# Kernel tuning notes

Hardware: AMD Instinct MI355X
Metric: run time of the kernel (lower is better)

Reference implementation:

```python
import jax, jax.numpy as jnp
import numpy as np

N = 8192      # nodes
R = 3         # relations
D_IN = 64
D_HID = 64
D_OUT = 64


def setup_inputs() -> dict:
    key = jax.random.key(0)
    ks = jax.random.split(key, 6)
    x = jax.random.normal(ks[0], (N, D_IN), dtype=jnp.float32)
    # dense normalized adjacency-hat per relation; 1/N scale keeps tanh unsaturated
    adj = jax.random.uniform(ks[1], (R, N, N), dtype=jnp.float32) * (1.0 / N)
    s1 = 1.0 / np.sqrt(D_IN)
    s2 = 1.0 / np.sqrt(D_HID)
    W1 = jax.random.uniform(ks[2], (R, D_IN, D_HID), dtype=jnp.float32, minval=-s1, maxval=s1)
    b1 = jax.random.uniform(ks[3], (R, D_HID), dtype=jnp.float32, minval=-s1, maxval=s1)
    W2 = jax.random.uniform(ks[4], (R, D_HID, D_OUT), dtype=jnp.float32, minval=-s2, maxval=s2)
    b2 = jax.random.uniform(ks[5], (R, D_OUT), dtype=jnp.float32, minval=-s2, maxval=s2)
    return {"x": x, "adj": adj, "W1": W1, "b1": b1, "W2": W2, "b2": b2}


def _relgcn_conv(x, adj, W, b):
    # per-relation linear: [R, N, d_out]
    h = jnp.einsum('nf,rfh->rnh', x, W) + b[:, None, :]
    # adjacency matmul per relation, summed over relations: [N, d_out]
    m = jnp.einsum('rnm,rmh->nh', adj, h)
    return jnp.tanh(m)


def reference(x, adj, W1, b1, W2, b2):
    h = _relgcn_conv(x, adj, W1, b1)   # layer 0: in -> hidden
    y = _relgcn_conv(h, adj, W2, b2)   # layer 1: hidden -> out
    return y
```

## Files before the change

### kernel.cpp

```cpp
#include <hip/hip_runtime.h>


#define NN 8192
#define TS 516

typedef __attribute__((ext_vector_type(4))) float float4v;
typedef __attribute__((ext_vector_type(8))) short short8v;
typedef __attribute__((ext_vector_type(4))) int int4v;

__device__ inline unsigned short f2bf(float f) {
  unsigned int u = __builtin_bit_cast(unsigned int, f);
  return (unsigned short)((u + 0x7FFFu + ((u >> 16) & 1u)) >> 16);
}

__device__ inline float tri_dither(unsigned int e) {
  unsigned int s = e * 2654435761u;
  s ^= s >> 16;
  s *= 2246822519u;
  s ^= s >> 13;
  return ((float)((s & 0xffffu) + (s >> 16)) * (1.f / 65536.f)) - 1.f;
}

__global__ __launch_bounds__(256) void prep(
    const float* __restrict__ in, const float* __restrict__ W,
    const float* __restrict__ b, unsigned short* __restrict__ hbf) {
  __shared__ float Ws[64 * 64];
  const int tid = threadIdx.x;
  const int r = blockIdx.x >> 8;
  const int g = blockIdx.x & 255;
  const int ml = tid >> 3;
  const int j0 = (tid & 7) * 8;
  const int m = g * 32 + ml;
#pragma unroll
  for (int i = 0; i < 16; ++i) Ws[tid + i * 256] = W[r * 4096 + tid + i * 256];
  float4v xr[16];
#pragma unroll
  for (int i = 0; i < 16; ++i) xr[i] = *(const float4v*)&in[(size_t)m * 64 + i * 4];
  float acc[8];
  {
    const float4v b0 = *(const float4v*)&b[r * 64 + j0];
    const float4v b1 = *(const float4v*)&b[r * 64 + j0 + 4];
#pragma unroll
    for (int jj = 0; jj < 4; ++jj) { acc[jj] = b0[jj]; acc[jj + 4] = b1[jj]; }
  }
  __syncthreads();
#pragma unroll
  for (int fi = 0; fi < 16; ++fi) {
    const float4v xv = xr[fi];
#pragma unroll
    for (int df = 0; df < 4; ++df) {
      const int f = fi * 4 + df;
      const float a = xv[df];
      const float4v w0 = *(const float4v*)&Ws[f * 64 + j0];
      const float4v w1 = *(const float4v*)&Ws[f * 64 + j0 + 4];
#pragma unroll
      for (int jj = 0; jj < 4; ++jj) {
        acc[jj] += a * w0[jj];
        acc[jj + 4] += a * w1[jj];
      }
    }
  }
  const size_t base = ((size_t)(r * 1024 + (m >> 3)) * 64) * 8 + (m & 7);
#pragma unroll
  for (int jj = 0; jj < 8; ++jj)
    hbf[base + (size_t)(j0 + jj) * 8] = f2bf(acc[jj]);
}

__global__ __launch_bounds__(256) void prep_q(
    const float* __restrict__ in, const float* __restrict__ W,
    const float* __restrict__ b, unsigned char* __restrict__ hq, float S) {
  __shared__ float Ws[64 * 64];
  const int tid = threadIdx.x;
  const int r = blockIdx.x >> 8;
  const int g = blockIdx.x & 255;
  const int ml = tid >> 3;
  const int j0 = (tid & 7) * 8;
  const int m = g * 32 + ml;
#pragma unroll
  for (int i = 0; i < 16; ++i) Ws[tid + i * 256] = W[r * 4096 + tid + i * 256];
  float4v xr[16];
#pragma unroll
  for (int i = 0; i < 16; ++i) xr[i] = *(const float4v*)&in[(size_t)m * 64 + i * 4];
  float acc[8];
  {
    const float4v b0 = *(const float4v*)&b[r * 64 + j0];
    const float4v b1 = *(const float4v*)&b[r * 64 + j0 + 4];
#pragma unroll
    for (int jj = 0; jj < 4; ++jj) { acc[jj] = b0[jj]; acc[jj + 4] = b1[jj]; }
  }
  __syncthreads();
#pragma unroll
  for (int fi = 0; fi < 16; ++fi) {
    const float4v xv = xr[fi];
#pragma unroll
    for (int df = 0; df < 4; ++df) {
      const int f = fi * 4 + df;
      const float a = xv[df];
      const float4v w0 = *(const float4v*)&Ws[f * 64 + j0];
      const float4v w1 = *(const float4v*)&Ws[f * 64 + j0 + 4];
#pragma unroll
      for (int jj = 0; jj < 4; ++jj) {
        acc[jj] += a * w0[jj];
        acc[jj + 4] += a * w1[jj];
      }
    }
  }
  const size_t base = ((size_t)(r * 1024 + (m >> 3)) * 64) * 8 + (m & 7);
#pragma unroll
  for (int jj = 0; jj < 8; ++jj) {
    float v = acc[jj] * S + tri_dither((unsigned)((r * NN + m) * 64 + j0 + jj));
    int q = (int)rintf(v);
    q = q > 127 ? 127 : (q < -127 ? -127 : q);
    hq[base + (size_t)(j0 + jj) * 8] = (unsigned char)(q & 0xff);
  }
}

__global__ __launch_bounds__(256) void gemm1_emit(
    const float* __restrict__ adj, const unsigned short* __restrict__ hbf,
    float* __restrict__ out, unsigned char* __restrict__ adjq) {
  __shared__ float lds[2 * 16 * TS];
  float* buf0 = lds;
  float* buf1 = lds + 16 * TS;
  const int tid = threadIdx.x;
  const int w = tid >> 6;
  const int l = tid & 63;
  const int lrow = l & 15;
  const int lk = l >> 4;
  const int mb = blockIdx.x;
  const int phase = (mb * 29) % 48;
  const int srow = tid >> 4;
  const int sseg = tid & 15;
  const float* arow = adj + (size_t)(mb * 16 + srow) * NN + sseg * 4;
  unsigned char* a8row = adjq + (size_t)(mb * 16 + srow) * NN + sseg * 4;

  float4v acc0 = {0.f, 0.f, 0.f, 0.f}, acc1 = acc0, acc2 = acc0, acc3 = acc0;
  float4v P0, P1, P2, P3, P4, P5, P6, P7, Q0, Q1, Q2, Q3, Q4, Q5, Q6, Q7;

#define TW(TQ) ((TQ) + phase >= 48 ? (TQ) + phase - 48 : (TQ) + phase)
#define TOFF(T) (((size_t)((T) >> 4) << 26) + ((size_t)((T) & 15) << 9))

#define GLOAD(T, S)                                                            \
  do {                                                                         \
    const float* pa_ = arow + TOFF(T);                                         \
    S##0 = __builtin_nontemporal_load((const float4v*)(pa_));                  \
    S##1 = __builtin_nontemporal_load((const float4v*)(pa_ + 64));             \
    S##2 = __builtin_nontemporal_load((const float4v*)(pa_ + 128));            \
    S##3 = __builtin_nontemporal_load((const float4v*)(pa_ + 192));            \
    S##4 = __builtin_nontemporal_load((const float4v*)(pa_ + 256));            \
    S##5 = __builtin_nontemporal_load((const float4v*)(pa_ + 320));            \
    S##6 = __builtin_nontemporal_load((const float4v*)(pa_ + 384));            \
    S##7 = __builtin_nontemporal_load((const float4v*)(pa_ + 448));            \
  } while (0)

#define Q8ST(S, K)                                                             \
  *(unsigned int*)(q8_ + (K) * 64) =                                           \
      (unsigned)(S[0] * 1040384.f + 0.5f) |                                    \
      ((unsigned)(S[1] * 1040384.f + 0.5f) << 8) |                             \
      ((unsigned)(S[2] * 1040384.f + 0.5f) << 16) |                            \
      ((unsigned)(S[3] * 1040384.f + 0.5f) << 24)

#define DSWRITE(BUF, S, T8)                                                    \
  do {                                                                         \
    float* p_ = (BUF) + srow * TS + sseg * 4;                                  \
    *(float4v*)(p_) = S##0;                                                    \
    *(float4v*)(p_ + 64) = S##1;                                               \
    *(float4v*)(p_ + 128) = S##2;                                              \
    *(float4v*)(p_ + 192) = S##3;                                              \
    *(float4v*)(p_ + 256) = S##4;                                              \
    *(float4v*)(p_ + 320) = S##5;                                              \
    *(float4v*)(p_ + 384) = S##6;                                              \
    *(float4v*)(p_ + 448) = S##7;                                              \
    unsigned char* q8_ = a8row + (T8);                                         \
    Q8ST(S##0, 0); Q8ST(S##1, 1); Q8ST(S##2, 2); Q8ST(S##3, 3);                \
    Q8ST(S##4, 4); Q8ST(S##5, 5); Q8ST(S##6, 6); Q8ST(S##7, 7);                \
  } while (0)

#define DO_CHUNK(CUR, CC, B0, B1, B2, B3)                                      \
  do {                                                                         \
    const float* ap_ = (CUR) + lrow * TS + (w * 4 + (CC)) * 32 + lk * 8;       \
    const float4v a0_ = *(const float4v*)ap_;                                  \
    const float4v a1_ = *(const float4v*)(ap_ + 4);                            \
    short8v av_;                                                               \
    av_[0] = (short)f2bf(a0_[0]); av_[1] = (short)f2bf(a0_[1]);                \
    av_[2] = (short)f2bf(a0_[2]); av_[3] = (short)f2bf(a0_[3]);                \
    av_[4] = (short)f2bf(a1_[0]); av_[5] = (short)f2bf(a1_[1]);                \
    av_[6] = (short)f2bf(a1_[2]); av_[7] = (short)f2bf(a1_[3]);                \
    acc0 = __builtin_amdgcn_mfma_f32_16x16x32_bf16(av_, B0, acc0, 0, 0, 0);    \
    acc1 = __builtin_amdgcn_mfma_f32_16x16x32_bf16(av_, B1, acc1, 0, 0, 0);    \
    acc2 = __builtin_amdgcn_mfma_f32_16x16x32_bf16(av_, B2, acc2, 0, 0, 0);    \
    acc3 = __builtin_amdgcn_mfma_f32_16x16x32_bf16(av_, B3, acc3, 0, 0, 0);    \
  } while (0)

#define TILE(TQ, CBUF, WBUF, WS, LS)                                           \
  do {                                                                         \
    const int T_ = TW(TQ);                                                     \
    const unsigned short* pbb_ =                                               \
        hbf +                                                                  \
        ((size_t)((T_ >> 4) * 1024 + (T_ & 15) * 64 + w * 16 + lk) * 512) +    \
        lrow * 8;                                                              \
    const short8v B00 = *(const short8v*)(pbb_);                               \
    const short8v B01 = *(const short8v*)(pbb_ + 128);                         \
    const short8v B02 = *(const short8v*)(pbb_ + 256);                         \
    const short8v B03 = *(const short8v*)(pbb_ + 384);                         \
    const short8v B10 = *(const short8v*)(pbb_ + 2048);                        \
    const short8v B11 = *(const short8v*)(pbb_ + 2176);                        \
    const short8v B12 = *(const short8v*)(pbb_ + 2304);                        \
    const short8v B13 = *(const short8v*)(pbb_ + 2432);                        \
    const short8v B20 = *(const short8v*)(pbb_ + 4096);                        \
    const short8v B21 = *(const short8v*)(pbb_ + 4224);                        \
    const short8v B22 = *(const short8v*)(pbb_ + 4352);                        \
    const short8v B23 = *(const short8v*)(pbb_ + 4480);                        \
    const short8v B30 = *(const short8v*)(pbb_ + 6144);                        \
    const short8v B31 = *(const short8v*)(pbb_ + 6272);                        \
    const short8v B32 = *(const short8v*)(pbb_ + 6400);                        \
    const short8v B33 = *(const short8v*)(pbb_ + 6528);                        \
    if ((TQ) + 1 < 48) DSWRITE(WBUF, WS, TOFF(TW((TQ) + 1)));                  \
    if ((TQ) + 2 < 48) GLOAD(TW((TQ) + 2), LS);                                \
    DO_CHUNK(CBUF, 0, B00, B01, B02, B03);                                     \
    DO_CHUNK(CBUF, 1, B10, B11, B12, B13);                                     \
    DO_CHUNK(CBUF, 2, B20, B21, B22, B23);                                     \
    DO_CHUNK(CBUF, 3, B30, B31, B32, B33);                                     \
    __syncthreads();                                                           \
  } while (0)

  GLOAD(TW(0), P);
  DSWRITE(buf0, P, TOFF(TW(0)));
  GLOAD(TW(1), Q);
  __syncthreads();

#pragma unroll 1
  for (int tq = 0; tq < 48; tq += 2) {
    TILE(tq, buf0, buf1, Q, P);
    TILE(tq + 1, buf1, buf0, P, Q);
  }
#undef TILE
#undef DO_CHUNK
#undef DSWRITE
#undef Q8ST
#undef GLOAD
#undef TW

  float* red = lds;
#pragma unroll
  for (int q = 0; q < 4; ++q) {
    red[w * 1024 + (lk * 4 + q) * 64 + 0 + lrow] = acc0[q];
    red[w * 1024 + (lk * 4 + q) * 64 + 16 + lrow] = acc1[q];
    red[w * 1024 + (lk * 4 + q) * 64 + 32 + lrow] = acc2[q];
    red[w * 1024 + (lk * 4 + q) * 64 + 48 + lrow] = acc3[q];
  }
  __syncthreads();
#pragma unroll
  for (int idx = tid; idx < 1024; idx += 256) {
    const float s = red[idx] + red[1024 + idx] + red[2048 + idx] + red[3072 + idx];
    out[(size_t)mb * 1024 + idx] = tanhf(s);
  }
}

__global__ __launch_bounds__(512) void gemm2_i8(
    const unsigned char* __restrict__ adjq, const unsigned char* __restrict__ hq,
    float* __restrict__ out, float inv) {
  __shared__ int red[8 * 1024];
  const int tid = threadIdx.x;
  const int w = tid >> 6;
  const int l = tid & 63;
  const int lrow = l & 15;
  const int lk = l >> 4;
  const int mb = blockIdx.x;
  const int poff = (mb * 29) % 96;
  const unsigned char* parow = adjq + (size_t)(mb * 16 + lrow) * NN + lk * 8;

  int4v acc0 = {0, 0, 0, 0}, acc1 = acc0, acc2 = acc0, acc3 = acc0;
  long pA, qA, sA;
  long pB0, pB1, pB2, pB3, qB0, qB1, qB2, qB3, sB0, sB1, sB2, sB3;

#define TW96(IT) ((IT) + poff >= 96 ? (IT) + poff - 96 : (IT) + poff)

#define ISSUE(IT, A, B0, B1, B2, B3)                                           \
  do {                                                                         \
    const int c_ = TW96(IT) * 8 + w;                                           \
    const int r_ = c_ >> 8;                                                    \
    const int mm_ = (c_ & 255) << 5;                                           \
    A = *(const long*)(parow + ((size_t)r_ << 26) + mm_);                      \
    const unsigned char* pb_ =                                                 \
        hq + (size_t)(r_ * 1024 + (mm_ >> 3) + lk) * 512 + lrow * 8;           \
    B0 = *(const long*)(pb_);                                                  \
    B1 = *(const long*)(pb_ + 128);                                            \
    B2 = *(const long*)(pb_ + 256);                                            \
    B3 = *(const long*)(pb_ + 384);                                            \
  } while (0)

#define COMPUTE(A, B0, B1, B2, B3)                                             \
  do {                                                                         \
    acc0 = __builtin_amdgcn_mfma_i32_16x16x32_i8(A, B0, acc0, 0, 0, 0);        \
    acc1 = __builtin_amdgcn_mfma_i32_16x16x32_i8(A, B1, acc1, 0, 0, 0);        \
    acc2 = __builtin_amdgcn_mfma_i32_16x16x32_i8(A, B2, acc2, 0, 0, 0);        \
    acc3 = __builtin_amdgcn_mfma_i32_16x16x32_i8(A, B3, acc3, 0, 0, 0);        \
  } while (0)

  ISSUE(0, pA, pB0, pB1, pB2, pB3);
  ISSUE(1, qA, qB0, qB1, qB2, qB3);
#pragma unroll 1
  for (int it = 0; it < 96; it += 3) {
    ISSUE(it + 2, sA, sB0, sB1, sB2, sB3);
    COMPUTE(pA, pB0, pB1, pB2, pB3);
    if (it + 3 < 96) ISSUE(it + 3, pA, pB0, pB1, pB2, pB3);
    COMPUTE(qA, qB0, qB1, qB2, qB3);
    if (it + 4 < 96) ISSUE(it + 4, qA, qB0, qB1, qB2, qB3);
    COMPUTE(sA, sB0, sB1, sB2, sB3);
  }
#undef ISSUE
#undef COMPUTE
#undef TW96

#pragma unroll
  for (int q = 0; q < 4; ++q) {
    red[w * 1024 + (lk * 4 + q) * 64 + 0 + lrow] = acc0[q];
    red[w * 1024 + (lk * 4 + q) * 64 + 16 + lrow] = acc1[q];
    red[w * 1024 + (lk * 4 + q) * 64 + 32 + lrow] = acc2[q];
    red[w * 1024 + (lk * 4 + q) * 64 + 48 + lrow] = acc3[q];
  }
  __syncthreads();
#pragma unroll
  for (int idx = tid; idx < 1024; idx += 512) {
    int s = 0;
#pragma unroll
    for (int wb = 0; wb < 8; ++wb) s += red[wb * 1024 + idx];
    out[(size_t)mb * 1024 + idx] = tanhf((float)s * inv);
  }
}

__global__ __launch_bounds__(256) void fill_sentinel(float* __restrict__ dst) {
  dst[blockIdx.x * 256 + threadIdx.x] = 7.0f;
}

extern "C" void kernel_launch(void* const* d_in, const int* in_sizes, int n_in,
                              void* d_out, int out_size, void* d_ws, size_t ws_size,
                              hipStream_t stream) {
  const float* x   = (const float*)d_in[0];
  const float* adj = (const float*)d_in[1];
  const float* W1  = (const float*)d_in[2];
  const float* b1  = (const float*)d_in[3];
  const float* W2  = (const float*)d_in[4];
  const float* b2  = (const float*)d_in[5];
  float* out = (float*)d_out;

  const size_t A8_B  = (size_t)3 * 8192 * 8192;
  const size_t HBF_B = (size_t)3 * 8192 * 64 * 2;
  const size_t T_B   = (size_t)8192 * 64 * 4;
  const size_t HQ_B  = (size_t)3 * 8192 * 64;
  if (ws_size < A8_B + HBF_B + T_B + HQ_B) {
    fill_sentinel<<<2048, 256, 0, stream>>>(out);
    return;
  }
  unsigned char* adjq = (unsigned char*)d_ws;
  unsigned short* hbf = (unsigned short*)((char*)d_ws + A8_B);
  float* t            = (float*)((char*)d_ws + A8_B + HBF_B);
  unsigned char* hq   = (unsigned char*)((char*)d_ws + A8_B + HBF_B + T_B);

  prep<<<3 * 256, 256, 0, stream>>>(x, W1, b1, hbf);
  gemm1_emit<<<512, 256, 0, stream>>>(adj, hbf, t, adjq);
  prep_q<<<3 * 256, 256, 0, stream>>>(t, W2, b2, hq, 64.f);
  gemm2_i8<<<512, 512, 0, stream>>>(adjq, hq, out, 1.f / (1040384.f * 64.f));
}
```

Measured before the change: 317.3 us.

## Switch layer-2 int8 GEMM to 16x16x64 MFMA with a fragment-tiled layout

Rewrites the quantized adjacency and hidden-feature layouts into 16-byte MFMA fragment tiles, so gemm2 can issue 128-bit loads and use the 16x16x64 i8 MFMA, halving its loop trip count. The gemm1 emit step now writes adjq in this tiled order. It also adds a single-block probe kernel that checks the new MFMA operand layout against a scalar reference and deliberately stalls if they disagree, which adds an extra launch and a serial dependency.

```diff
diff --git a/kernel.cpp b/kernel.cpp
--- a/kernel.cpp
+++ b/kernel.cpp
@@ -105,13 +105,13 @@
       }
     }
   }
-  const size_t base = ((size_t)(r * 1024 + (m >> 3)) * 64) * 8 + (m & 7);
+  const size_t base = ((size_t)(r * 512 + (m >> 4)) * 64) * 16 + (m & 15);
 #pragma unroll
   for (int jj = 0; jj < 8; ++jj) {
     float v = acc[jj] * S + tri_dither((unsigned)((r * NN + m) * 64 + j0 + jj));
     int q = (int)rintf(v);
     q = q > 127 ? 127 : (q < -127 ? -127 : q);
-    hq[base + (size_t)(j0 + jj) * 8] = (unsigned char)(q & 0xff);
+    hq[base + (size_t)(j0 + jj) * 16] = (unsigned char)(q & 0xff);
   }
 }
 
@@ -131,7 +131,8 @@
   const int srow = tid >> 4;
   const int sseg = tid & 15;
   const float* arow = adj + (size_t)(mb * 16 + srow) * NN + sseg * 4;
-  unsigned char* a8row = adjq + (size_t)(mb * 16 + srow) * NN + sseg * 4;
+  unsigned char* a8base = adjq + (size_t)mb * 384 * 1024 +
+                          (size_t)(srow + 16 * (sseg >> 2)) * 16 + (sseg & 3) * 4;
 
   float4v acc0 = {0.f, 0.f, 0.f, 0.f}, acc1 = acc0, acc2 = acc0, acc3 = acc0;
   float4v P0, P1, P2, P3, P4, P5, P6, P7, Q0, Q1, Q2, Q3, Q4, Q5, Q6, Q7;
@@ -152,14 +153,13 @@
     S##7 = __builtin_nontemporal_load((const float4v*)(pa_ + 448));            \
   } while (0)
 
-#define Q8ST(S, K)                                                             \
-  *(unsigned int*)(q8_ + (K) * 64) =                                           \
-      (unsigned)(S[0] * 1040384.f + 0.5f) |                                    \
-      ((unsigned)(S[1] * 1040384.f + 0.5f) << 8) |                             \
-      ((unsigned)(S[2] * 1040384.f + 0.5f) << 16) |                            \
-      ((unsigned)(S[3] * 1040384.f + 0.5f) << 24)
-
-#define DSWRITE(BUF, S, T8)                                                    \
+#define QPK(S)                                                                 \
+  ((unsigned)(S[0] * 1040384.f + 0.5f) |                                       \
+   ((unsigned)(S[1] * 1040384.f + 0.5f) << 8) |                                \
+   ((unsigned)(S[2] * 1040384.f + 0.5f) << 16) |                               \
+   ((unsigned)(S[3] * 1040384.f + 0.5f) << 24))
+
+#define DSWRITE(BUF, S, T_)                                                    \
   do {                                                                         \
     float* p_ = (BUF) + srow * TS + sseg * 4;                                  \
     *(float4v*)(p_) = S##0;                                                    \
@@ -170,9 +170,16 @@
     *(float4v*)(p_ + 320) = S##5;                                              \
     *(float4v*)(p_ + 384) = S##6;                                              \
     *(float4v*)(p_ + 448) = S##7;                                              \
-    unsigned char* q8_ = a8row + (T8);                                         \
-    Q8ST(S##0, 0); Q8ST(S##1, 1); Q8ST(S##2, 2); Q8ST(S##3, 3);                \
-    Q8ST(S##4, 4); Q8ST(S##5, 5); Q8ST(S##6, 6); Q8ST(S##7, 7);                \
+    unsigned char* q8_ =                                                       \
+        a8base + ((size_t)((T_ >> 4) * 128 + (T_ & 15) * 8)) * 1024;           \
+    *(unsigned*)(q8_) = QPK(S##0);                                             \
+    *(unsigned*)(q8_ + 1024) = QPK(S##1);                                      \
+    *(unsigned*)(q8_ + 2048) = QPK(S##2);                                      \
+    *(unsigned*)(q8_ + 3072) = QPK(S##3);                                      \
+    *(unsigned*)(q8_ + 4096) = QPK(S##4);                                      \
+    *(unsigned*)(q8_ + 5120) = QPK(S##5);                                      \
+    *(unsigned*)(q8_ + 6144) = QPK(S##6);                                      \
+    *(unsigned*)(q8_ + 7168) = QPK(S##7);                                      \
   } while (0)
 
 #define DO_CHUNK(CUR, CC, B0, B1, B2, B3)                                      \
@@ -214,7 +221,7 @@
     const short8v B31 = *(const short8v*)(pbb_ + 6272);                        \
     const short8v B32 = *(const short8v*)(pbb_ + 6400);                        \
     const short8v B33 = *(const short8v*)(pbb_ + 6528);                        \
-    if ((TQ) + 1 < 48) DSWRITE(WBUF, WS, TOFF(TW((TQ) + 1)));                  \
+    if ((TQ) + 1 < 48) DSWRITE(WBUF, WS, TW((TQ) + 1));                        \
     if ((TQ) + 2 < 48) GLOAD(TW((TQ) + 2), LS);                                \
     DO_CHUNK(CBUF, 0, B00, B01, B02, B03);                                     \
     DO_CHUNK(CBUF, 1, B10, B11, B12, B13);                                     \
@@ -224,7 +231,7 @@
   } while (0)
 
   GLOAD(TW(0), P);
-  DSWRITE(buf0, P, TOFF(TW(0)));
+  DSWRITE(buf0, P, TW(0));
   GLOAD(TW(1), Q);
   __syncthreads();
 
@@ -236,7 +243,7 @@
 #undef TILE
 #undef DO_CHUNK
 #undef DSWRITE
-#undef Q8ST
+#undef QPK
 #undef GLOAD
 #undef TW
 
@@ -266,51 +273,50 @@
   const int lrow = l & 15;
   const int lk = l >> 4;
   const int mb = blockIdx.x;
-  const int poff = (mb * 29) % 96;
-  const unsigned char* parow = adjq + (size_t)(mb * 16 + lrow) * NN + lk * 8;
+  const int poff = (mb * 29) % 48;
+  const unsigned char* pabase = adjq + (size_t)mb * 384 * 1024 + l * 16;
 
   int4v acc0 = {0, 0, 0, 0}, acc1 = acc0, acc2 = acc0, acc3 = acc0;
-  long pA, qA, sA;
-  long pB0, pB1, pB2, pB3, qB0, qB1, qB2, qB3, sB0, sB1, sB2, sB3;
-
-#define TW96(IT) ((IT) + poff >= 96 ? (IT) + poff - 96 : (IT) + poff)
+  int4v pA, pB0, pB1, pB2, pB3, qA, qB0, qB1, qB2, qB3, sA, sB0, sB1, sB2, sB3;
+
+#define TW48(IT) ((IT) + poff >= 48 ? (IT) + poff - 48 : (IT) + poff)
 
 #define ISSUE(IT, A, B0, B1, B2, B3)                                           \
   do {                                                                         \
-    const int c_ = TW96(IT) * 8 + w;                                           \
-    const int r_ = c_ >> 8;                                                    \
-    const int mm_ = (c_ & 255) << 5;                                           \
-    A = *(const long*)(parow + ((size_t)r_ << 26) + mm_);                      \
+    const int c_ = TW48(IT) * 8 + w;                  \
+    A = *(const int4v*)(pabase + (size_t)c_ * 1024);                           \
+    const int r_ = c_ >> 7;                                                    \
+    const int mm_ = (c_ & 127) << 6;                                           \
     const unsigned char* pb_ =                                                 \
-        hq + (size_t)(r_ * 1024 + (mm_ >> 3) + lk) * 512 + lrow * 8;           \
-    B0 = *(const long*)(pb_);                                                  \
-    B1 = *(const long*)(pb_ + 128);                                            \
-    B2 = *(const long*)(pb_ + 256);                                            \
-    B3 = *(const long*)(pb_ + 384);                                            \
+        hq + ((size_t)(r_ * 512 + (mm_ >> 4) + lk) * 64 + lrow) * 16;          \
+    B0 = *(const int4v*)(pb_);                                                 \
+    B1 = *(const int4v*)(pb_ + 256);                                           \
+    B2 = *(const int4v*)(pb_ + 512);                                           \
+    B3 = *(const int4v*)(pb_ + 768);                                           \
   } while (0)
 
 #define COMPUTE(A, B0, B1, B2, B3)                                             \
   do {                                                                         \
-    acc0 = __builtin_amdgcn_mfma_i32_16x16x32_i8(A, B0, acc0, 0, 0, 0);        \
-    acc1 = __builtin_amdgcn_mfma_i32_16x16x32_i8(A, B1, acc1, 0, 0, 0);        \
-    acc2 = __builtin_amdgcn_mfma_i32_16x16x32_i8(A, B2, acc2, 0, 0, 0);        \
-    acc3 = __builtin_amdgcn_mfma_i32_16x16x32_i8(A, B3, acc3, 0, 0, 0);        \
+    acc0 = __builtin_amdgcn_mfma_i32_16x16x64_i8(A, B0, acc0, 0, 0, 0);        \
+    acc1 = __builtin_amdgcn_mfma_i32_16x16x64_i8(A, B1, acc1, 0, 0, 0);        \
+    acc2 = __builtin_amdgcn_mfma_i32_16x16x64_i8(A, B2, acc2, 0, 0, 0);        \
+    acc3 = __builtin_amdgcn_mfma_i32_16x16x64_i8(A, B3, acc3, 0, 0, 0);        \
   } while (0)
 
   ISSUE(0, pA, pB0, pB1, pB2, pB3);
   ISSUE(1, qA, qB0, qB1, qB2, qB3);
 #pragma unroll 1
-  for (int it = 0; it < 96; it += 3) {
+  for (int it = 0; it < 48; it += 3) {
     ISSUE(it + 2, sA, sB0, sB1, sB2, sB3);
     COMPUTE(pA, pB0, pB1, pB2, pB3);
-    if (it + 3 < 96) ISSUE(it + 3, pA, pB0, pB1, pB2, pB3);
+    if (it + 3 < 48) ISSUE(it + 3, pA, pB0, pB1, pB2, pB3);
     COMPUTE(qA, qB0, qB1, qB2, qB3);
-    if (it + 4 < 96) ISSUE(it + 4, qA, qB0, qB1, qB2, qB3);
+    if (it + 4 < 48) ISSUE(it + 4, qA, qB0, qB1, qB2, qB3);
     COMPUTE(sA, sB0, sB1, sB2, sB3);
   }
 #undef ISSUE
 #undef COMPUTE
-#undef TW96
+#undef TW48
 
 #pragma unroll
   for (int q = 0; q < 4; ++q) {
@@ -326,6 +332,54 @@
 #pragma unroll
     for (int wb = 0; wb < 8; ++wb) s += red[wb * 1024 + idx];
     out[(size_t)mb * 1024 + idx] = tanhf((float)s * inv);
+  }
+}
+
+__global__ __launch_bounds__(64) void i8_probe(
+    const unsigned char* __restrict__ adjq, const unsigned char* __restrict__ hq) {
+  __shared__ int cm[16 * 64];
+  __shared__ int flag;
+  const int l = threadIdx.x;
+  if (l == 0) flag = 0;
+  const int lrow = l & 15, lk = l >> 4;
+  int4v acc[4];
+#pragma unroll
+  for (int g = 0; g < 4; ++g) acc[g] = (int4v){0, 0, 0, 0};
+#pragma unroll
+  for (int c = 0; c < 2; ++c) {
+    const int4v av = *(const int4v*)&adjq[((size_t)c * 64 + l) * 16];
+#pragma unroll
+    for (int g = 0; g < 4; ++g) {
+      const int4v bv =
+          *(const int4v*)&hq[((size_t)(c * 4 + lk) * 64 + g * 16 + lrow) * 16];
+      acc[g] = __builtin_amdgcn_mfma_i32_16x16x64_i8(av, bv, acc[g], 0, 0, 0);
+    }
+  }
+#pragma unroll
+  for (int g = 0; g < 4; ++g)
+#pragma unroll
+    for (int q = 0; q < 4; ++q)
+      cm[(lk * 4 + q) * 64 + g * 16 + lrow] = acc[g][q];
+  __syncthreads();
+  const int row = l & 15, c0 = (l >> 4) * 16;
+  int bad = 0;
+  for (int cc = 0; cc < 16; ++cc) {
+    const int col = c0 + cc;
+    int ref = 0;
+    for (int k = 0; k < 128; ++k) {
+      const unsigned char a8 =
+          adjq[((size_t)(k >> 6) * 64 + (row & 15) + 16 * ((k >> 4) & 3)) * 16 +
+               (k & 15)];
+      const unsigned char h8 =
+          hq[((size_t)(k >> 4) * 64 + col) * 16 + (k & 15)];
+      ref += (int)a8 * (int)(signed char)h8;
+    }
+    if (cm[row * 64 + col] != ref) bad = 1;
+  }
+  if (bad) atomicOr(&flag, 1);
+  __syncthreads();
+  if (flag) {
+    for (int i = 0; i < 150; ++i) __builtin_amdgcn_s_sleep(127);
   }
 }
 
@@ -360,5 +414,6 @@
   prep<<<3 * 256, 256, 0, stream>>>(x, W1, b1, hbf);
   gemm1_emit<<<512, 256, 0, stream>>>(adj, hbf, t, adjq);
   prep_q<<<3 * 256, 256, 0, stream>>>(t, W2, b2, hq, 64.f);
+  i8_probe<<<1, 64, 0, stream>>>(adjq, hq);
   gemm2_i8<<<512, 512, 0, stream>>>(adjq, hq, out, 1.f / (1040384.f * 64.f));
 }
```

New measurement: 373.2 us. +17.6%, slower.

## Split gemm2 K dimension across two blocks and reduce with tanh finisher

Applied to the files above, without the earlier changes.

The int8 second-layer GEMM now splits the reduction over relations and columns into two halves, launching 1024 blocks instead of 512 so more CUs stay busy. Each block writes int32 partial sums to a workspace buffer, and a new elementwise kernel adds the two halves and applies the scale and tanh. The software pipeline also deepens from three to four in-flight load stages. The cost is an extra kernel launch, an extra 4 MB of partial-sum traffic, and more registers per thread.

```diff
diff --git a/kernel.cpp b/kernel.cpp
--- a/kernel.cpp
+++ b/kernel.cpp
@@ -258,26 +258,28 @@
 
 __global__ __launch_bounds__(512) void gemm2_i8(
     const unsigned char* __restrict__ adjq, const unsigned char* __restrict__ hq,
-    float* __restrict__ out, float inv) {
+    int* __restrict__ part) {
   __shared__ int red[8 * 1024];
   const int tid = threadIdx.x;
   const int w = tid >> 6;
   const int l = tid & 63;
   const int lrow = l & 15;
   const int lk = l >> 4;
-  const int mb = blockIdx.x;
-  const int poff = (mb * 29) % 96;
+  const int mb = blockIdx.x >> 1;
+  const int kh = blockIdx.x & 1;
+  const int poff = (mb * 29) % 48;
   const unsigned char* parow = adjq + (size_t)(mb * 16 + lrow) * NN + lk * 8;
 
   int4v acc0 = {0, 0, 0, 0}, acc1 = acc0, acc2 = acc0, acc3 = acc0;
-  long pA, qA, sA;
-  long pB0, pB1, pB2, pB3, qB0, qB1, qB2, qB3, sB0, sB1, sB2, sB3;
-
-#define TW96(IT) ((IT) + poff >= 96 ? (IT) + poff - 96 : (IT) + poff)
+  long pA, qA, sA, uA;
+  long pB0, pB1, pB2, pB3, qB0, qB1, qB2, qB3;
+  long sB0, sB1, sB2, sB3, uB0, uB1, uB2, uB3;
+
+#define TW48(IT) ((IT) + poff >= 48 ? (IT) + poff - 48 : (IT) + poff)
 
 #define ISSUE(IT, A, B0, B1, B2, B3)                                           \
   do {                                                                         \
-    const int c_ = TW96(IT) * 8 + w;                                           \
+    const int c_ = TW48(IT) * 8 + w + kh * 384;                                \
     const int r_ = c_ >> 8;                                                    \
     const int mm_ = (c_ & 255) << 5;                                           \
     A = *(const long*)(parow + ((size_t)r_ << 26) + mm_);                      \
@@ -299,18 +301,21 @@
 
   ISSUE(0, pA, pB0, pB1, pB2, pB3);
   ISSUE(1, qA, qB0, qB1, qB2, qB3);
+  ISSUE(2, sA, sB0, sB1, sB2, sB3);
 #pragma unroll 1
-  for (int it = 0; it < 96; it += 3) {
-    ISSUE(it + 2, sA, sB0, sB1, sB2, sB3);
+  for (int it = 0; it < 48; it += 4) {
+    ISSUE(it + 3, uA, uB0, uB1, uB2, uB3);
     COMPUTE(pA, pB0, pB1, pB2, pB3);
-    if (it + 3 < 96) ISSUE(it + 3, pA, pB0, pB1, pB2, pB3);
+    if (it + 4 < 48) ISSUE(it + 4, pA, pB0, pB1, pB2, pB3);
     COMPUTE(qA, qB0, qB1, qB2, qB3);
-    if (it + 4 < 96) ISSUE(it + 4, qA, qB0, qB1, qB2, qB3);
+    if (it + 5 < 48) ISSUE(it + 5, qA, qB0, qB1, qB2, qB3);
     COMPUTE(sA, sB0, sB1, sB2, sB3);
+    if (it + 6 < 48) ISSUE(it + 6, sA, sB0, sB1, sB2, sB3);
+    COMPUTE(uA, uB0, uB1, uB2, uB3);
   }
 #undef ISSUE
 #undef COMPUTE
-#undef TW96
+#undef TW48
 
 #pragma unroll
   for (int q = 0; q < 4; ++q) {
@@ -325,8 +330,15 @@
     int s = 0;
 #pragma unroll
     for (int wb = 0; wb < 8; ++wb) s += red[wb * 1024 + idx];
-    out[(size_t)mb * 1024 + idx] = tanhf((float)s * inv);
-  }
+    part[(size_t)kh * (8192 * 64) + (size_t)mb * 1024 + idx] = s;
+  }
+}
+
+__global__ __launch_bounds__(256) void finish_tanh_i32(
+    const int* __restrict__ part, float* __restrict__ dst, float inv) {
+  const int i = blockIdx.x * 256 + threadIdx.x;
+  const int s = part[i] + part[i + 8192 * 64];
+  dst[i] = tanhf((float)s * inv);
 }
 
 __global__ __launch_bounds__(256) void fill_sentinel(float* __restrict__ dst) {
@@ -348,7 +360,8 @@
   const size_t HBF_B = (size_t)3 * 8192 * 64 * 2;
   const size_t T_B   = (size_t)8192 * 64 * 4;
   const size_t HQ_B  = (size_t)3 * 8192 * 64;
-  if (ws_size < A8_B + HBF_B + T_B + HQ_B) {
+  const size_t P_B   = (size_t)2 * 8192 * 64 * 4;
+  if (ws_size < A8_B + HBF_B + T_B + HQ_B + P_B) {
     fill_sentinel<<<2048, 256, 0, stream>>>(out);
     return;
   }
@@ -356,9 +369,11 @@
   unsigned short* hbf = (unsigned short*)((char*)d_ws + A8_B);
   float* t            = (float*)((char*)d_ws + A8_B + HBF_B);
   unsigned char* hq   = (unsigned char*)((char*)d_ws + A8_B + HBF_B + T_B);
+  int* part           = (int*)((char*)d_ws + A8_B + HBF_B + T_B + HQ_B);
 
   prep<<<3 * 256, 256, 0, stream>>>(x, W1, b1, hbf);
   gemm1_emit<<<512, 256, 0, stream>>>(adj, hbf, t, adjq);
   prep_q<<<3 * 256, 256, 0, stream>>>(t, W2, b2, hq, 64.f);
-  gemm2_i8<<<512, 512, 0, stream>>>(adjq, hq, out, 1.f / (1040384.f * 64.f));
-}
+  gemm2_i8<<<1024, 512, 0, stream>>>(adjq, hq, part);
+  finish_tanh_i32<<<2048, 256, 0, stream>>>(part, out, 1.f / (1040384.f * 64.f));
+}
```

Result: no change. 318.8 us (+0.5%).
